# Optimization experiments

Hardware: AMD Instinct MI355X
Metric: run time of the kernel (lower is better)

## Reference

```python
import jax, jax.numpy as jnp
import numpy as np

EMB = 64
HID = 1024
SEQ = 9
BATCH = 4096


def setup_inputs() -> dict:
    key = jax.random.key(0)
    ks = jax.random.split(key, 10)
    s = lambda *sh: 1.0 / np.sqrt(sh[-1])
    return {
        "observed": jax.random.normal(ks[0], (SEQ, BATCH, 2), dtype=jnp.float32),
        "W_emb": jax.random.normal(ks[1], (EMB, 2), dtype=jnp.float32) * s(2),
        "b_emb": jnp.zeros((EMB,), dtype=jnp.float32),
        "W_ih": jax.random.normal(ks[2], (4 * HID, EMB), dtype=jnp.float32) * s(EMB),
        "b_ih": jnp.zeros((4 * HID,), dtype=jnp.float32),
        "W_hh": jax.random.normal(ks[3], (4 * HID, HID), dtype=jnp.float32) * s(HID),
        "b_hh": jnp.zeros((4 * HID,), dtype=jnp.float32),
        "W_out": jax.random.normal(ks[4], (5, HID), dtype=jnp.float32) * s(HID),
        "b_out": jnp.zeros((5,), dtype=jnp.float32),
        "n_predict": 12,
    }


def _cell(x, h, c, W_ih, b_ih, W_hh, b_hh):
    # torch.nn.LSTMCell gate math, gate order i, f, g, o
    gates = x @ W_ih.T + b_ih + h @ W_hh.T + b_hh  # [B, 4H]
    i, f, g, o = jnp.split(gates, 4, axis=-1)
    c_new = jax.nn.sigmoid(f) * c + jax.nn.sigmoid(i) * jnp.tanh(g)
    h_new = jax.nn.sigmoid(o) * jnp.tanh(c_new)
    return h_new, c_new


def reference(observed, W_emb, b_emb, W_ih, b_ih, W_hh, b_hh, W_out, b_out, n_predict):
    B = observed.shape[1]
    H = W_hh.shape[1]
    h0 = jnp.zeros((B, H), dtype=observed.dtype)
    c0 = jnp.zeros((B, H), dtype=observed.dtype)

    diffs = observed[1:] - observed[:-1]  # [SEQ-1, B, 2]

    def obs_step(carry, d):
        h, c = carry
        emb = jax.nn.relu(d @ W_emb.T + b_emb)  # [B, EMB]
        h, c = _cell(emb, h, c, W_ih, b_ih, W_hh, b_hh)
        normal = h @ W_out.T + b_out  # [B, 5]
        return (h, c), normal

    (h, c), normals_obs = jax.lax.scan(obs_step, (h0, c0), diffs)
    new_vel = normals_obs[-1][:, :2]

    def pred_step(carry, _):
        h, c, nv = carry
        emb = jax.nn.relu(jax.lax.stop_gradient(nv) @ W_emb.T + b_emb)
        h, c = _cell(emb, h, c, W_ih, b_ih, W_hh, b_hh)
        normal = h @ W_out.T + b_out
        return (h, c, normal[:, :2]), normal

    (_, _, _), normals_pred = jax.lax.scan(
        pred_step, (h, c, new_vel), None, length=n_predict - 1)

    # training-mode output: stacked raw 'normal' params, shape [SEQ-1+n_predict-1, B, 5]
    return jnp.concatenate([normals_obs, normals_pred], axis=0)
```

## Files before the change

kernel.cpp:

```cpp
#include <hip/hip_runtime.h>
#include <stdint.h>
#include <stddef.h>

#define BATCH 4096
#define HID   1024
#define EMB   64
#define KDIM  1088
#define NSTEP 19
#define NOBS  8

#define BM 128
#define BN 128
#define BK 32

typedef _Float16 f16;
typedef _Float16 half8 __attribute__((ext_vector_type(8)));
typedef float    float4v __attribute__((ext_vector_type(4)));

__device__ __forceinline__ float sigm(float x) { return 1.f / (1.f + __expf(-x)); }
__device__ __forceinline__ float tanh_f(float x) { return 1.f - 2.f / (__expf(2.f * x) + 1.f); }

__device__ __forceinline__ void gload_lds16(const void* gp, void* lp) {
  __builtin_amdgcn_global_load_lds(
      (const __attribute__((address_space(1))) uint32_t*)gp,
      (__attribute__((address_space(3))) uint32_t*)lp, 16, 0, 0);
}

__global__ void pack_kernel(const float* __restrict__ W_ih, const float* __restrict__ b_ih,
                            const float* __restrict__ W_hh, const float* __restrict__ b_hh,
                            f16* __restrict__ Wc, float* __restrict__ bc) {
  int gid = blockIdx.x * blockDim.x + threadIdx.x;
  int p = gid / KDIM;
  int k = gid - p * KDIM;
  int t = p >> 7;
  int g = (p >> 5) & 3;
  int u = p & 31;
  int orig = g * HID + t * 32 + u;
  float v = (k < EMB) ? W_ih[orig * EMB + k] : W_hh[orig * HID + (k - EMB)];
  Wc[gid] = (f16)v;
  if (k == 0) bc[p] = b_ih[orig] + b_hh[orig];
}

__global__ void emb0_kernel(const float* __restrict__ observed,
                            const float* __restrict__ W_emb, const float* __restrict__ b_emb,
                            f16* __restrict__ Xc) {
  int gid = blockIdx.x * blockDim.x + threadIdx.x;
  int b = gid >> 6, j = gid & 63;
  const float* o0 = observed + b * 2;
  const float* o1 = o0 + BATCH * 2;
  float d0 = o1[0] - o0[0];
  float d1 = o1[1] - o0[1];
  float v = d0 * W_emb[2 * j] + d1 * W_emb[2 * j + 1] + b_emb[j];
  Xc[(size_t)b * KDIM + j] = (f16)fmaxf(v, 0.f);
}

__global__ __launch_bounds__(256, 4)
void gemm_cell_kernel(const f16* __restrict__ Xc, const f16* __restrict__ Wc,
                      const float* __restrict__ bc,
                      float* __restrict__ c_ws, f16* __restrict__ Xn,
                      const float* __restrict__ obs_next, int do_emb,
                      const float* __restrict__ W_emb, const float* __restrict__ b_emb) {
  __shared__ f16 smem[2 * BM * BK];
  const int tid = threadIdx.x;
  const int lane = tid & 63;
  const int w = tid >> 6;
  const int l15 = lane & 15;
  const int quad = lane >> 4;
  const int bm = blockIdx.y, bn = blockIdx.x;

  float4v acc[2][8];
#pragma unroll
  for (int mi = 0; mi < 2; ++mi)
#pragma unroll
    for (int ni = 0; ni < 8; ++ni)
      acc[mi][ni] = (float4v){0.f, 0.f, 0.f, 0.f};

  int a_off[2], b_off[8];
#pragma unroll
  for (int mi = 0; mi < 2; ++mi) {
    int r = w * 32 + mi * 16 + l15;
    a_off[mi] = r * 32 + (quad ^ ((r >> 1) & 3)) * 8;
  }
#pragma unroll
  for (int ni = 0; ni < 8; ++ni) {
    int r = ni * 16 + l15;
    b_off[ni] = BM * BK + r * 32 + (quad ^ ((r >> 1) & 3)) * 8;
  }

  for (int kt = 0; kt < KDIM / BK; ++kt) {
    const int k0 = kt * BK;
    __syncthreads();
#pragma unroll
    for (int cph = 0; cph < 2; ++cph) {
      int s = tid + cph * 256;
      int r = s >> 2;
      int cl = (s & 3) ^ ((r >> 1) & 3);
      const f16* ga = Xc + (size_t)(bm * BM + r) * KDIM + k0 + cl * 8;
      const f16* gb = Wc + (size_t)(bn * BN + r) * KDIM + k0 + cl * 8;
      uint32_t lbase = (uint32_t)(w * 64 + cph * 256) * 16;
      gload_lds16(ga, (char*)smem + lbase);
      gload_lds16(gb, (char*)smem + 8192 + lbase);
    }
    __syncthreads();

    half8 af[2];
#pragma unroll
    for (int mi = 0; mi < 2; ++mi) af[mi] = *(const half8*)(smem + a_off[mi]);
#pragma unroll
    for (int g4 = 0; g4 < 2; ++g4) {
      half8 bf[4];
#pragma unroll
      for (int i = 0; i < 4; ++i) bf[i] = *(const half8*)(smem + b_off[g4 * 4 + i]);
#pragma unroll
      for (int mi = 0; mi < 2; ++mi)
#pragma unroll
        for (int i = 0; i < 4; ++i)
          acc[mi][g4 * 4 + i] =
              __builtin_amdgcn_mfma_f32_16x16x32_f16(af[mi], bf[i], acc[mi][g4 * 4 + i], 0, 0, 0);
    }
  }

  float bias[8];
#pragma unroll
  for (int ni = 0; ni < 8; ++ni) bias[ni] = bc[bn * BN + ni * 16 + l15];

  float* cbase = c_ws + ((size_t)(blockIdx.y * 32 + blockIdx.x) * 256 + tid) * 16;
  float4v cv[4];
#pragma unroll
  for (int q = 0; q < 4; ++q) cv[q] = *(const float4v*)(cbase + q * 4);

#pragma unroll
  for (int mi = 0; mi < 2; ++mi) {
#pragma unroll
    for (int u16 = 0; u16 < 2; ++u16) {
      const int j = bn * 32 + u16 * 16 + l15;
      const int ci = mi * 2 + u16;
#pragma unroll
      for (int r = 0; r < 4; ++r) {
        const int brow = bm * BM + w * 32 + mi * 16 + quad * 4 + r;
        float gi = acc[mi][u16 + 0][r] + bias[u16 + 0];
        float gf = acc[mi][u16 + 2][r] + bias[u16 + 2];
        float gg = acc[mi][u16 + 4][r] + bias[u16 + 4];
        float go = acc[mi][u16 + 6][r] + bias[u16 + 6];
        float cn = sigm(gf) * cv[ci][r] + sigm(gi) * tanh_f(gg);
        cv[ci][r] = cn;
        float h = sigm(go) * tanh_f(cn);
        Xn[(size_t)brow * KDIM + EMB + j] = (f16)h;
      }
    }
  }
#pragma unroll
  for (int q = 0; q < 4; ++q) *(float4v*)(cbase + q * 4) = cv[q];

  if (do_emb && bn == 0) {
    const int row = bm * BM + (tid >> 1);
    const int jb = (tid & 1) * 32;
    const float* o0 = obs_next + row * 2;
    const float* o1 = o0 + BATCH * 2;
    float d0 = o1[0] - o0[0];
    float d1 = o1[1] - o0[1];
    f16* dst = Xn + (size_t)row * KDIM + jb;
#pragma unroll
    for (int jj = 0; jj < 32; ++jj) {
      int j = jb + jj;
      float v = d0 * W_emb[2 * j] + d1 * W_emb[2 * j + 1] + b_emb[j];
      dst[jj] = (f16)fmaxf(v, 0.f);
    }
  }
}

__global__ __launch_bounds__(256)
void outemb_kernel(const f16* __restrict__ Xh, const float* __restrict__ W_out,
                   const float* __restrict__ b_out, float* __restrict__ out_t,
                   int emb_flag, const float* __restrict__ W_emb,
                   const float* __restrict__ b_emb, f16* __restrict__ Xn) {
  __shared__ float s_nv[8][2];
  const int tid = threadIdx.x;
  const int lane = tid & 63;
  const int w = tid >> 6;
  const int row0 = blockIdx.x * 8;

#pragma unroll
  for (int rr = 0; rr < 2; ++rr) {
    const int row = row0 + w * 2 + rr;
    const f16* hrow = Xh + (size_t)row * KDIM + EMB;
    half8 h0 = *(const half8*)(hrow + lane * 16);
    half8 h1 = *(const half8*)(hrow + lane * 16 + 8);
    float a[5];
#pragma unroll
    for (int o = 0; o < 5; ++o) {
      const float* wo = W_out + o * HID + lane * 16;
      float s = 0.f;
#pragma unroll
      for (int e = 0; e < 8; ++e) s += (float)h0[e] * wo[e];
#pragma unroll
      for (int e = 0; e < 8; ++e) s += (float)h1[e] * wo[8 + e];
      a[o] = s;
    }
#pragma unroll
    for (int sh = 32; sh > 0; sh >>= 1)
#pragma unroll
      for (int o = 0; o < 5; ++o) a[o] += __shfl_down(a[o], sh, 64);
    if (lane == 0) {
#pragma unroll
      for (int o = 0; o < 5; ++o) out_t[(size_t)row * 5 + o] = a[o] + b_out[o];
      s_nv[w * 2 + rr][0] = a[0] + b_out[0];
      s_nv[w * 2 + rr][1] = a[1] + b_out[1];
    }
  }

  if (emb_flag) {
    __syncthreads();
    for (int s = tid; s < 512; s += 256) {
      int rr = s >> 6, jc = s & 63;
      int row = row0 + rr;
      float d0 = s_nv[rr][0], d1 = s_nv[rr][1];
      float v = d0 * W_emb[2 * jc] + d1 * W_emb[2 * jc + 1] + b_emb[jc];
      Xn[(size_t)row * KDIM + jc] = (f16)fmaxf(v, 0.f);
    }
  }
}

extern "C" void kernel_launch(void* const* d_in, const int* in_sizes, int n_in,
                              void* d_out, int out_size, void* d_ws, size_t ws_size,
                              hipStream_t stream) {
  const float* observed = (const float*)d_in[0];
  const float* W_emb = (const float*)d_in[1];
  const float* b_emb = (const float*)d_in[2];
  const float* W_ih = (const float*)d_in[3];
  const float* b_ih = (const float*)d_in[4];
  const float* W_hh = (const float*)d_in[5];
  const float* b_hh = (const float*)d_in[6];
  const float* W_out = (const float*)d_in[7];
  const float* b_out = (const float*)d_in[8];
  float* out = (float*)d_out;

  uint8_t* ws = (uint8_t*)d_ws;
  const size_t WC_BYTES = (size_t)4096 * KDIM * sizeof(f16);
  f16* Wc = (f16*)ws;
  float* bc = (float*)(ws + WC_BYTES);
  f16* X0 = (f16*)(ws + WC_BYTES + 16384);
  f16* X1 = (f16*)(ws + 2 * WC_BYTES + 16384);
  float* c_ws = (float*)(ws + 3 * WC_BYTES + 16384);

  pack_kernel<<<(4096 * KDIM) / 256, 256, 0, stream>>>(W_ih, b_ih, W_hh, b_hh, Wc, bc);
  hipMemsetAsync(X0, 0, WC_BYTES, stream);
  hipMemsetAsync(c_ws, 0, (size_t)BATCH * HID * 4, stream);
  emb0_kernel<<<(BATCH * EMB) / 256, 256, 0, stream>>>(observed, W_emb, b_emb, X0);

  for (int t = 0; t < NSTEP; ++t) {
    f16* Xc = (t & 1) ? X1 : X0;
    f16* Xn = (t & 1) ? X0 : X1;
    const int do_emb = (t + 1 < NOBS) ? 1 : 0;
    dim3 grid(BATCH / BN, BATCH / BM);
    gemm_cell_kernel<<<grid, 256, 0, stream>>>(
        Xc, Wc, bc, c_ws, Xn, observed + (size_t)(t + 1) * BATCH * 2, do_emb, W_emb, b_emb);
    const int emb_pred = (t >= 7 && t + 1 < NSTEP) ? 1 : 0;
    outemb_kernel<<<BATCH / 8, 256, 0, stream>>>(
        Xn, W_out, b_out, out + (size_t)t * BATCH * 5, emb_pred, W_emb, b_emb, Xn);
  }
}
```

Measured before the change: 1.297 ms.

## Enlarge GEMM tile to 128x256 with register-staged double-buffered LDS pipeline

Doubles the N tile so each 4-wave block computes a 128x256 output with a 2x2 wave layout and 4x8 MFMA accumulators per wave. It also replaces direct global-to-LDS loads with register-staged prefetch into a double-buffered LDS, leaving one barrier per K step. The goal is more operand reuse and overlap of global loads with MFMA work. In exchange it uses more registers and LDS, cuts occupancy to 2 blocks per CU, and halves the grid's N dimension, which the launch code not shown must match.

Result: faster. 1.234 ms (-4.8%).

```diff
diff --git a/kernel.cpp b/kernel.cpp
--- a/kernel.cpp
+++ b/kernel.cpp
@@ -10,21 +10,19 @@
 #define NOBS  8
 
 #define BM 128
-#define BN 128
+#define BN 256
 #define BK 32
+#define BUFH 12288
 
 typedef _Float16 f16;
 typedef _Float16 half8 __attribute__((ext_vector_type(8)));
 typedef float    float4v __attribute__((ext_vector_type(4)));
+typedef int      int4v   __attribute__((ext_vector_type(4)));
 
 __device__ __forceinline__ float sigm(float x) { return 1.f / (1.f + __expf(-x)); }
 __device__ __forceinline__ float tanh_f(float x) { return 1.f - 2.f / (__expf(2.f * x) + 1.f); }
 
-__device__ __forceinline__ void gload_lds16(const void* gp, void* lp) {
-  __builtin_amdgcn_global_load_lds(
-      (const __attribute__((address_space(1))) uint32_t*)gp,
-      (__attribute__((address_space(3))) uint32_t*)lp, 16, 0, 0);
-}
+#define KBAR() asm volatile("s_waitcnt lgkmcnt(0)\n\ts_barrier" ::: "memory")
 
 __global__ void pack_kernel(const float* __restrict__ W_ih, const float* __restrict__ b_ih,
                             const float* __restrict__ W_hh, const float* __restrict__ b_hh,
@@ -54,90 +52,138 @@
   Xc[(size_t)b * KDIM + j] = (f16)fmaxf(v, 0.f);
 }
 
-__global__ __launch_bounds__(256, 4)
+__global__ __launch_bounds__(256, 2)
 void gemm_cell_kernel(const f16* __restrict__ Xc, const f16* __restrict__ Wc,
                       const float* __restrict__ bc,
                       float* __restrict__ c_ws, f16* __restrict__ Xn,
                       const float* __restrict__ obs_next, int do_emb,
                       const float* __restrict__ W_emb, const float* __restrict__ b_emb) {
-  __shared__ f16 smem[2 * BM * BK];
+  __shared__ f16 smem[2 * BUFH];
   const int tid = threadIdx.x;
   const int lane = tid & 63;
   const int w = tid >> 6;
   const int l15 = lane & 15;
   const int quad = lane >> 4;
-  const int bm = blockIdx.y, bn = blockIdx.x;
-
-  float4v acc[2][8];
-#pragma unroll
-  for (int mi = 0; mi < 2; ++mi)
-#pragma unroll
-    for (int ni = 0; ni < 8; ++ni)
-      acc[mi][ni] = (float4v){0.f, 0.f, 0.f, 0.f};
-
-  int a_off[2], b_off[8];
-#pragma unroll
-  for (int mi = 0; mi < 2; ++mi) {
-    int r = w * 32 + mi * 16 + l15;
-    a_off[mi] = r * 32 + (quad ^ ((r >> 1) & 3)) * 8;
+  const int bm = blockIdx.y;
+  const int bnB = blockIdx.x;
+  const int wM = w & 1;
+  const int wN = w >> 1;
+  const int tt = bnB * 2 + wN;
+
+  int sA0 = tid, sA1 = tid + 256;
+  int rA0 = sA0 >> 2, cA0 = (sA0 & 3) ^ ((rA0 >> 1) & 3);
+  int rA1 = sA1 >> 2, cA1 = (sA1 & 3) ^ ((rA1 >> 1) & 3);
+  const f16* gA0 = Xc + (size_t)(bm * BM + rA0) * KDIM + cA0 * 8;
+  const f16* gA1 = Xc + (size_t)(bm * BM + rA1) * KDIM + cA1 * 8;
+  const int lA0 = sA0 * 8, lA1 = sA1 * 8;
+
+  const f16* gB[4];
+  int lB[4];
+#pragma unroll
+  for (int h = 0; h < 4; ++h) {
+    int s = tid + h * 256;
+    int r = s >> 2, cl = (s & 3) ^ ((r >> 1) & 3);
+    gB[h] = Wc + (size_t)(bnB * BN + r) * KDIM + cl * 8;
+    lB[h] = 4096 + s * 8;
+  }
+
+  int a_off[4], b_off[8];
+#pragma unroll
+  for (int mi = 0; mi < 4; ++mi) {
+    int r = wM * 64 + mi * 16 + l15;
+    a_off[mi] = r * 32 + ((quad ^ ((r >> 1) & 3)) * 8);
   }
 #pragma unroll
   for (int ni = 0; ni < 8; ++ni) {
-    int r = ni * 16 + l15;
-    b_off[ni] = BM * BK + r * 32 + (quad ^ ((r >> 1) & 3)) * 8;
-  }
+    int r = wN * 128 + ni * 16 + l15;
+    b_off[ni] = 4096 + r * 32 + ((quad ^ ((r >> 1) & 3)) * 8);
+  }
+
+  float4v acc[4][8];
+#pragma unroll
+  for (int mi = 0; mi < 4; ++mi)
+#pragma unroll
+    for (int ni = 0; ni < 8; ++ni) acc[mi][ni] = (float4v){0.f, 0.f, 0.f, 0.f};
+
+  int4v va0 = *(const int4v*)gA0;
+  int4v va1 = *(const int4v*)gA1;
+  int4v vb0 = *(const int4v*)gB[0];
+  int4v vb1 = *(const int4v*)gB[1];
+  int4v vb2 = *(const int4v*)gB[2];
+  int4v vb3 = *(const int4v*)gB[3];
+  *(int4v*)(smem + lA0) = va0;
+  *(int4v*)(smem + lA1) = va1;
+  *(int4v*)(smem + lB[0]) = vb0;
+  *(int4v*)(smem + lB[1]) = vb1;
+  *(int4v*)(smem + lB[2]) = vb2;
+  *(int4v*)(smem + lB[3]) = vb3;
+  va0 = *(const int4v*)(gA0 + BK);
+  va1 = *(const int4v*)(gA1 + BK);
+  vb0 = *(const int4v*)(gB[0] + BK);
+  vb1 = *(const int4v*)(gB[1] + BK);
+  vb2 = *(const int4v*)(gB[2] + BK);
+  vb3 = *(const int4v*)(gB[3] + BK);
+  KBAR();
 
   for (int kt = 0; kt < KDIM / BK; ++kt) {
-    const int k0 = kt * BK;
-    __syncthreads();
-#pragma unroll
-    for (int cph = 0; cph < 2; ++cph) {
-      int s = tid + cph * 256;
-      int r = s >> 2;
-      int cl = (s & 3) ^ ((r >> 1) & 3);
-      const f16* ga = Xc + (size_t)(bm * BM + r) * KDIM + k0 + cl * 8;
-      const f16* gb = Wc + (size_t)(bn * BN + r) * KDIM + k0 + cl * 8;
-      uint32_t lbase = (uint32_t)(w * 64 + cph * 256) * 16;
-      gload_lds16(ga, (char*)smem + lbase);
-      gload_lds16(gb, (char*)smem + 8192 + lbase);
-    }
-    __syncthreads();
-
-    half8 af[2];
-#pragma unroll
-    for (int mi = 0; mi < 2; ++mi) af[mi] = *(const half8*)(smem + a_off[mi]);
+    const f16* sb = smem + (kt & 1) * BUFH;
+    f16* so = smem + ((kt + 1) & 1) * BUFH;
+
+    if (kt + 1 < KDIM / BK) {
+      *(int4v*)(so + lA0) = va0;
+      *(int4v*)(so + lA1) = va1;
+      *(int4v*)(so + lB[0]) = vb0;
+      *(int4v*)(so + lB[1]) = vb1;
+      *(int4v*)(so + lB[2]) = vb2;
+      *(int4v*)(so + lB[3]) = vb3;
+      if (kt + 2 < KDIM / BK) {
+        const int off = (kt + 2) * BK;
+        va0 = *(const int4v*)(gA0 + off);
+        va1 = *(const int4v*)(gA1 + off);
+        vb0 = *(const int4v*)(gB[0] + off);
+        vb1 = *(const int4v*)(gB[1] + off);
+        vb2 = *(const int4v*)(gB[2] + off);
+        vb3 = *(const int4v*)(gB[3] + off);
+      }
+    }
+
+    half8 af[4];
+#pragma unroll
+    for (int mi = 0; mi < 4; ++mi) af[mi] = *(const half8*)(sb + a_off[mi]);
 #pragma unroll
     for (int g4 = 0; g4 < 2; ++g4) {
       half8 bf[4];
 #pragma unroll
-      for (int i = 0; i < 4; ++i) bf[i] = *(const half8*)(smem + b_off[g4 * 4 + i]);
-#pragma unroll
-      for (int mi = 0; mi < 2; ++mi)
+      for (int i = 0; i < 4; ++i) bf[i] = *(const half8*)(sb + b_off[g4 * 4 + i]);
+#pragma unroll
+      for (int mi = 0; mi < 4; ++mi)
 #pragma unroll
         for (int i = 0; i < 4; ++i)
           acc[mi][g4 * 4 + i] =
               __builtin_amdgcn_mfma_f32_16x16x32_f16(af[mi], bf[i], acc[mi][g4 * 4 + i], 0, 0, 0);
     }
+
+    if (kt + 1 < KDIM / BK) KBAR();
   }
 
   float bias[8];
 #pragma unroll
-  for (int ni = 0; ni < 8; ++ni) bias[ni] = bc[bn * BN + ni * 16 + l15];
-
-  float* cbase = c_ws + ((size_t)(blockIdx.y * 32 + blockIdx.x) * 256 + tid) * 16;
-  float4v cv[4];
-#pragma unroll
-  for (int q = 0; q < 4; ++q) cv[q] = *(const float4v*)(cbase + q * 4);
-
-#pragma unroll
-  for (int mi = 0; mi < 2; ++mi) {
+  for (int ni = 0; ni < 8; ++ni) bias[ni] = bc[tt * 128 + ni * 16 + l15];
+
+  float* cbase = c_ws + ((size_t)(blockIdx.y * 16 + blockIdx.x) * 256 + tid) * 32;
+  float4v cv[8];
+#pragma unroll
+  for (int q = 0; q < 8; ++q) cv[q] = *(const float4v*)(cbase + q * 4);
+
+#pragma unroll
+  for (int mi = 0; mi < 4; ++mi) {
 #pragma unroll
     for (int u16 = 0; u16 < 2; ++u16) {
-      const int j = bn * 32 + u16 * 16 + l15;
+      const int j = tt * 32 + u16 * 16 + l15;
       const int ci = mi * 2 + u16;
 #pragma unroll
       for (int r = 0; r < 4; ++r) {
-        const int brow = bm * BM + w * 32 + mi * 16 + quad * 4 + r;
+        const int brow = bm * BM + wM * 64 + mi * 16 + quad * 4 + r;
         float gi = acc[mi][u16 + 0][r] + bias[u16 + 0];
         float gf = acc[mi][u16 + 2][r] + bias[u16 + 2];
         float gg = acc[mi][u16 + 4][r] + bias[u16 + 4];
@@ -150,9 +196,9 @@
     }
   }
 #pragma unroll
-  for (int q = 0; q < 4; ++q) *(float4v*)(cbase + q * 4) = cv[q];
-
-  if (do_emb && bn == 0) {
+  for (int q = 0; q < 8; ++q) *(float4v*)(cbase + q * 4) = cv[q];
+
+  if (do_emb && bnB == 0) {
     const int row = bm * BM + (tid >> 1);
     const int jb = (tid & 1) * 32;
     const float* o0 = obs_next + row * 2;
```

## Pre-swizzle operands into MFMA fragment layout and load directly to registers

Applied to the files above, without the earlier changes.

Weights and activations are stored in a fragment-major layout matching the 16x16x32 MFMA operand order. The GEMM then loads fragments straight from global memory into registers with a double-buffered register pipeline, with no LDS staging or barriers. Block tile grows to 256x128 with 4x8 accumulators per wave and occupancy hint 2. The output projection kernel is rewritten for the new layout, handling 16 rows per block with an LDS reduction. The risk is higher register pressure and uncoalesced-to-L2 reuse, since each wave refetches B fragments with no LDS sharing.

Result: faster. 1.100 ms (-15.2%).

```diff
diff --git a/kernel.cpp b/kernel.cpp
--- a/kernel.cpp
+++ b/kernel.cpp
@@ -6,12 +6,9 @@
 #define HID   1024
 #define EMB   64
 #define KDIM  1088
+#define NKT   34
 #define NSTEP 19
 #define NOBS  8
-
-#define BM 128
-#define BN 128
-#define BK 32
 
 typedef _Float16 f16;
 typedef _Float16 half8 __attribute__((ext_vector_type(8)));
@@ -20,30 +17,30 @@
 __device__ __forceinline__ float sigm(float x) { return 1.f / (1.f + __expf(-x)); }
 __device__ __forceinline__ float tanh_f(float x) { return 1.f - 2.f / (__expf(2.f * x) + 1.f); }
 
-__device__ __forceinline__ void gload_lds16(const void* gp, void* lp) {
-  __builtin_amdgcn_global_load_lds(
-      (const __attribute__((address_space(1))) uint32_t*)gp,
-      (__attribute__((address_space(3))) uint32_t*)lp, 16, 0, 0);
+__device__ __forceinline__ int xf_idx(int row, int k) {
+  return ((((row >> 4) * NKT + (k >> 5)) * 64) + (row & 15) + (((k >> 3) & 3) << 4)) * 8 + (k & 7);
 }
 
 __global__ void pack_kernel(const float* __restrict__ W_ih, const float* __restrict__ b_ih,
                             const float* __restrict__ W_hh, const float* __restrict__ b_hh,
-                            f16* __restrict__ Wc, float* __restrict__ bc) {
+                            f16* __restrict__ Wsw, float* __restrict__ bc) {
   int gid = blockIdx.x * blockDim.x + threadIdx.x;
-  int p = gid / KDIM;
-  int k = gid - p * KDIM;
-  int t = p >> 7;
-  int g = (p >> 5) & 3;
-  int u = p & 31;
+  int j = gid & 7;
+  int lane = (gid >> 3) & 63;
+  int c16 = (gid >> 9) & 255;
+  int kt = gid >> 17;
+  int p = c16 * 16 + (lane & 15);
+  int k = kt * 32 + ((lane >> 4) << 3) + j;
+  int t = p >> 7, g = (p >> 5) & 3, u = p & 31;
   int orig = g * HID + t * 32 + u;
-  float v = (k < EMB) ? W_ih[orig * EMB + k] : W_hh[orig * HID + (k - EMB)];
-  Wc[gid] = (f16)v;
+  float val = (k < EMB) ? W_ih[orig * EMB + k] : W_hh[orig * HID + (k - EMB)];
+  Wsw[gid] = (f16)val;
   if (k == 0) bc[p] = b_ih[orig] + b_hh[orig];
 }
 
 __global__ void emb0_kernel(const float* __restrict__ observed,
                             const float* __restrict__ W_emb, const float* __restrict__ b_emb,
-                            f16* __restrict__ Xc) {
+                            f16* __restrict__ Xf) {
   int gid = blockIdx.x * blockDim.x + threadIdx.x;
   int b = gid >> 6, j = gid & 63;
   const float* o0 = observed + b * 2;
@@ -51,93 +48,80 @@
   float d0 = o1[0] - o0[0];
   float d1 = o1[1] - o0[1];
   float v = d0 * W_emb[2 * j] + d1 * W_emb[2 * j + 1] + b_emb[j];
-  Xc[(size_t)b * KDIM + j] = (f16)fmaxf(v, 0.f);
-}
-
-__global__ __launch_bounds__(256, 4)
-void gemm_cell_kernel(const f16* __restrict__ Xc, const f16* __restrict__ Wc,
+  Xf[xf_idx(b, j)] = (f16)fmaxf(v, 0.f);
+}
+
+__global__ __launch_bounds__(256, 2)
+void gemm_cell_kernel(const f16* __restrict__ Xf, const f16* __restrict__ Wsw,
                       const float* __restrict__ bc,
                       float* __restrict__ c_ws, f16* __restrict__ Xn,
                       const float* __restrict__ obs_next, int do_emb,
                       const float* __restrict__ W_emb, const float* __restrict__ b_emb) {
-  __shared__ f16 smem[2 * BM * BK];
   const int tid = threadIdx.x;
   const int lane = tid & 63;
   const int w = tid >> 6;
   const int l15 = lane & 15;
   const int quad = lane >> 4;
-  const int bm = blockIdx.y, bn = blockIdx.x;
-
-  float4v acc[2][8];
-#pragma unroll
-  for (int mi = 0; mi < 2; ++mi)
-#pragma unroll
-    for (int ni = 0; ni < 8; ++ni)
-      acc[mi][ni] = (float4v){0.f, 0.f, 0.f, 0.f};
-
-  int a_off[2], b_off[8];
-#pragma unroll
-  for (int mi = 0; mi < 2; ++mi) {
-    int r = w * 32 + mi * 16 + l15;
-    a_off[mi] = r * 32 + (quad ^ ((r >> 1) & 3)) * 8;
-  }
-#pragma unroll
-  for (int ni = 0; ni < 8; ++ni) {
-    int r = ni * 16 + l15;
-    b_off[ni] = BM * BK + r * 32 + (quad ^ ((r >> 1) & 3)) * 8;
-  }
-
-  for (int kt = 0; kt < KDIM / BK; ++kt) {
-    const int k0 = kt * BK;
-    __syncthreads();
-#pragma unroll
-    for (int cph = 0; cph < 2; ++cph) {
-      int s = tid + cph * 256;
-      int r = s >> 2;
-      int cl = (s & 3) ^ ((r >> 1) & 3);
-      const f16* ga = Xc + (size_t)(bm * BM + r) * KDIM + k0 + cl * 8;
-      const f16* gb = Wc + (size_t)(bn * BN + r) * KDIM + k0 + cl * 8;
-      uint32_t lbase = (uint32_t)(w * 64 + cph * 256) * 16;
-      gload_lds16(ga, (char*)smem + lbase);
-      gload_lds16(gb, (char*)smem + 8192 + lbase);
-    }
-    __syncthreads();
-
-    half8 af[2];
-#pragma unroll
-    for (int mi = 0; mi < 2; ++mi) af[mi] = *(const half8*)(smem + a_off[mi]);
-#pragma unroll
-    for (int g4 = 0; g4 < 2; ++g4) {
-      half8 bf[4];
-#pragma unroll
-      for (int i = 0; i < 4; ++i) bf[i] = *(const half8*)(smem + b_off[g4 * 4 + i]);
-#pragma unroll
-      for (int mi = 0; mi < 2; ++mi)
-#pragma unroll
-        for (int i = 0; i < 4; ++i)
-          acc[mi][g4 * 4 + i] =
-              __builtin_amdgcn_mfma_f32_16x16x32_f16(af[mi], bf[i], acc[mi][g4 * 4 + i], 0, 0, 0);
-    }
-  }
+  const int tt = blockIdx.x;
+  const int mB = blockIdx.y;
+  const int rt0 = mB * 16 + w * 4;
+
+  const f16* aB = Xf + (size_t)rt0 * (NKT * 512) + lane * 8;
+  const f16* bB = Wsw + (size_t)tt * 8 * 512 + lane * 8;
+
+  float4v acc[4][8];
+#pragma unroll
+  for (int mi = 0; mi < 4; ++mi)
+#pragma unroll
+    for (int ni = 0; ni < 8; ++ni) acc[mi][ni] = (float4v){0.f, 0.f, 0.f, 0.f};
+
+  half8 afA[4], bfA[8], afB[4], bfB[8];
+
+#define LOADF(af, bf, kt)                                                          \
+  do {                                                                             \
+    _Pragma("unroll") for (int mi = 0; mi < 4; ++mi)                               \
+        af[mi] = *(const half8*)(aB + mi * (NKT * 512) + (kt) * 512);              \
+    _Pragma("unroll") for (int ni = 0; ni < 8; ++ni)                               \
+        bf[ni] = *(const half8*)(bB + ni * 512 + (kt) * 131072);                   \
+  } while (0)
+
+#define MFMA_ALL(af, bf)                                                           \
+  do {                                                                             \
+    _Pragma("unroll") for (int mi = 0; mi < 4; ++mi)                               \
+    _Pragma("unroll") for (int ni = 0; ni < 8; ++ni)                               \
+        acc[mi][ni] =                                                              \
+            __builtin_amdgcn_mfma_f32_16x16x32_f16(af[mi], bf[ni], acc[mi][ni], 0, 0, 0); \
+  } while (0)
+
+  LOADF(afA, bfA, 0);
+  for (int i = 0; i < NKT / 2; ++i) {
+    const int k1 = 2 * i + 1;
+    LOADF(afB, bfB, k1);
+    MFMA_ALL(afA, bfA);
+    if (k1 + 1 < NKT) LOADF(afA, bfA, k1 + 1);
+    MFMA_ALL(afB, bfB);
+  }
+#undef LOADF
+#undef MFMA_ALL
 
   float bias[8];
 #pragma unroll
-  for (int ni = 0; ni < 8; ++ni) bias[ni] = bc[bn * BN + ni * 16 + l15];
-
-  float* cbase = c_ws + ((size_t)(blockIdx.y * 32 + blockIdx.x) * 256 + tid) * 16;
-  float4v cv[4];
-#pragma unroll
-  for (int q = 0; q < 4; ++q) cv[q] = *(const float4v*)(cbase + q * 4);
-
-#pragma unroll
-  for (int mi = 0; mi < 2; ++mi) {
+  for (int ni = 0; ni < 8; ++ni) bias[ni] = bc[tt * 128 + ni * 16 + l15];
+
+  float* cbase = c_ws + ((size_t)(mB * 32 + tt) * 256 + tid) * 32;
+  float4v cv[8];
+#pragma unroll
+  for (int q = 0; q < 8; ++q) cv[q] = *(const float4v*)(cbase + q * 4);
+
+#pragma unroll
+  for (int mi = 0; mi < 4; ++mi) {
 #pragma unroll
     for (int u16 = 0; u16 < 2; ++u16) {
-      const int j = bn * 32 + u16 * 16 + l15;
+      const int j = tt * 32 + u16 * 16 + l15;
       const int ci = mi * 2 + u16;
 #pragma unroll
       for (int r = 0; r < 4; ++r) {
-        const int brow = bm * BM + w * 32 + mi * 16 + quad * 4 + r;
+        const int row = mB * 256 + w * 64 + mi * 16 + quad * 4 + r;
         float gi = acc[mi][u16 + 0][r] + bias[u16 + 0];
         float gf = acc[mi][u16 + 2][r] + bias[u16 + 2];
         float gg = acc[mi][u16 + 4][r] + bias[u16 + 4];
@@ -145,26 +129,23 @@
         float cn = sigm(gf) * cv[ci][r] + sigm(gi) * tanh_f(gg);
         cv[ci][r] = cn;
         float h = sigm(go) * tanh_f(cn);
-        Xn[(size_t)brow * KDIM + EMB + j] = (f16)h;
+        Xn[xf_idx(row, EMB + j)] = (f16)h;
       }
     }
   }
 #pragma unroll
-  for (int q = 0; q < 4; ++q) *(float4v*)(cbase + q * 4) = cv[q];
-
-  if (do_emb && bn == 0) {
-    const int row = bm * BM + (tid >> 1);
-    const int jb = (tid & 1) * 32;
+  for (int q = 0; q < 8; ++q) *(float4v*)(cbase + q * 4) = cv[q];
+
+  if (do_emb && tt == 0) {
+    const int row = mB * 256 + tid;
     const float* o0 = obs_next + row * 2;
     const float* o1 = o0 + BATCH * 2;
     float d0 = o1[0] - o0[0];
     float d1 = o1[1] - o0[1];
-    f16* dst = Xn + (size_t)row * KDIM + jb;
-#pragma unroll
-    for (int jj = 0; jj < 32; ++jj) {
-      int j = jb + jj;
+#pragma unroll
+    for (int j = 0; j < EMB; ++j) {
       float v = d0 * W_emb[2 * j] + d1 * W_emb[2 * j + 1] + b_emb[j];
-      dst[jj] = (f16)fmaxf(v, 0.f);
+      Xn[xf_idx(row, j)] = (f16)fmaxf(v, 0.f);
     }
   }
 }
@@ -174,49 +155,53 @@
                    const float* __restrict__ b_out, float* __restrict__ out_t,
                    int emb_flag, const float* __restrict__ W_emb,
                    const float* __restrict__ b_emb, f16* __restrict__ Xn) {
-  __shared__ float s_nv[8][2];
+  __shared__ float red[4][16][5];
+  __shared__ float s_nv[16][2];
   const int tid = threadIdx.x;
   const int lane = tid & 63;
   const int w = tid >> 6;
-  const int row0 = blockIdx.x * 8;
-
-#pragma unroll
-  for (int rr = 0; rr < 2; ++rr) {
-    const int row = row0 + w * 2 + rr;
-    const f16* hrow = Xh + (size_t)row * KDIM + EMB;
-    half8 h0 = *(const half8*)(hrow + lane * 16);
-    half8 h1 = *(const half8*)(hrow + lane * 16 + 8);
-    float a[5];
+  const int l15 = lane & 15;
+  const int quad = lane >> 4;
+  const int rt = blockIdx.x;
+
+  float a[5] = {0.f, 0.f, 0.f, 0.f, 0.f};
+#pragma unroll
+  for (int i = 0; i < 8; ++i) {
+    const int kt = 2 + w + 4 * i;
+    half8 hv = *(const half8*)(Xh + ((rt * NKT + kt) * 64 + lane) * 8);
+    const float* wo = W_out + kt * 32 + quad * 8 - EMB;
 #pragma unroll
     for (int o = 0; o < 5; ++o) {
-      const float* wo = W_out + o * HID + lane * 16;
+      const float* wp = wo + o * HID;
       float s = 0.f;
 #pragma unroll
-      for (int e = 0; e < 8; ++e) s += (float)h0[e] * wo[e];
-#pragma unroll
-      for (int e = 0; e < 8; ++e) s += (float)h1[e] * wo[8 + e];
-      a[o] = s;
-    }
-#pragma unroll
-    for (int sh = 32; sh > 0; sh >>= 1)
-#pragma unroll
-      for (int o = 0; o < 5; ++o) a[o] += __shfl_down(a[o], sh, 64);
-    if (lane == 0) {
-#pragma unroll
-      for (int o = 0; o < 5; ++o) out_t[(size_t)row * 5 + o] = a[o] + b_out[o];
-      s_nv[w * 2 + rr][0] = a[0] + b_out[0];
-      s_nv[w * 2 + rr][1] = a[1] + b_out[1];
-    }
-  }
-
+      for (int e = 0; e < 8; ++e) s += (float)hv[e] * wp[e];
+      a[o] += s;
+    }
+  }
+#pragma unroll
+  for (int o = 0; o < 5; ++o) {
+    a[o] += __shfl_xor(a[o], 16, 64);
+    a[o] += __shfl_xor(a[o], 32, 64);
+  }
+  if (quad == 0)
+#pragma unroll
+    for (int o = 0; o < 5; ++o) red[w][l15][o] = a[o];
+  __syncthreads();
+  if (tid < 80) {
+    const int row = tid / 5, o = tid - row * 5;
+    float v = red[0][row][o] + red[1][row][o] + red[2][row][o] + red[3][row][o] + b_out[o];
+    out_t[(size_t)(rt * 16 + row) * 5 + o] = v;
+    if (o < 2) s_nv[row][o] = v;
+  }
   if (emb_flag) {
     __syncthreads();
-    for (int s = tid; s < 512; s += 256) {
-      int rr = s >> 6, jc = s & 63;
-      int row = row0 + rr;
+    for (int s = tid; s < 1024; s += 256) {
+      const int rr = s >> 6, jc = s & 63;
+      const int row = rt * 16 + rr;
       float d0 = s_nv[rr][0], d1 = s_nv[rr][1];
       float v = d0 * W_emb[2 * jc] + d1 * W_emb[2 * jc + 1] + b_emb[jc];
-      Xn[(size_t)row * KDIM + jc] = (f16)fmaxf(v, 0.f);
+      Xn[xf_idx(row, jc)] = (f16)fmaxf(v, 0.f);
     }
   }
 }
@@ -237,13 +222,13 @@
 
   uint8_t* ws = (uint8_t*)d_ws;
   const size_t WC_BYTES = (size_t)4096 * KDIM * sizeof(f16);
-  f16* Wc = (f16*)ws;
+  f16* Wsw = (f16*)ws;
   float* bc = (float*)(ws + WC_BYTES);
   f16* X0 = (f16*)(ws + WC_BYTES + 16384);
   f16* X1 = (f16*)(ws + 2 * WC_BYTES + 16384);
   float* c_ws = (float*)(ws + 3 * WC_BYTES + 16384);
 
-  pack_kernel<<<(4096 * KDIM) / 256, 256, 0, stream>>>(W_ih, b_ih, W_hh, b_hh, Wc, bc);
+  pack_kernel<<<(4096 * KDIM) / 256, 256, 0, stream>>>(W_ih, b_ih, W_hh, b_hh, Wsw, bc);
   hipMemsetAsync(X0, 0, WC_BYTES, stream);
   hipMemsetAsync(c_ws, 0, (size_t)BATCH * HID * 4, stream);
   emb0_kernel<<<(BATCH * EMB) / 256, 256, 0, stream>>>(observed, W_emb, b_emb, X0);
@@ -252,11 +237,11 @@
     f16* Xc = (t & 1) ? X1 : X0;
     f16* Xn = (t & 1) ? X0 : X1;
     const int do_emb = (t + 1 < NOBS) ? 1 : 0;
-    dim3 grid(BATCH / BN, BATCH / BM);
+    dim3 grid(32, 16);
     gemm_cell_kernel<<<grid, 256, 0, stream>>>(
-        Xc, Wc, bc, c_ws, Xn, observed + (size_t)(t + 1) * BATCH * 2, do_emb, W_emb, b_emb);
+        Xc, Wsw, bc, c_ws, Xn, observed + (size_t)(t + 1) * BATCH * 2, do_emb, W_emb, b_emb);
     const int emb_pred = (t >= 7 && t + 1 < NSTEP) ? 1 : 0;
-    outemb_kernel<<<BATCH / 8, 256, 0, stream>>>(
+    outemb_kernel<<<BATCH / 16, 256, 0, stream>>>(
         Xn, W_out, b_out, out + (size_t)t * BATCH * 5, emb_pred, W_emb, b_emb, Xn);
   }
 }
```
